# Kernel optimization log

Measured on AMD Instinct MI355X. Metric: run time of the kernel, lower is better.

The kernel has to match this reference:

```python
import math
import jax, jax.numpy as jnp
import numpy as np

B, H, S, D = 2, 16, 2048, 64

def setup_inputs() -> dict:
    key = jax.random.key(0)
    kq, kk, kv = jax.random.split(key, 3)
    return {
        "query": jax.random.normal(kq, (B, H, S, D), dtype=jnp.float32),
        "key": jax.random.normal(kk, (B, H, S, D), dtype=jnp.float32),
        "value": jax.random.normal(kv, (B, H, S, D), dtype=jnp.float32),
        "mask": jnp.ones((B, S, 1), dtype=jnp.float32),  # padding mask, 1 = keep
        "mask_now": 0,  # 0 -> causal (tril diag=0); 1 -> strict causal (diag=-1)
    }

def reference(query, key, value, mask, mask_now):
    d_k = query.shape[-1]
    seq_len = mask.shape[1]
    # [B,H,S,S] scaled scores
    attn_scores = jnp.einsum("bhqd,bhkd->bhqk", query, key) / math.sqrt(d_k)
    diag = -1 if mask_now else 0
    triu_mask = jnp.tril(jnp.ones((seq_len, seq_len), dtype=mask.dtype), diag)  # [S,S]
    # mask[:, :, 0] -> per-query padding mask broadcast over key dim: [B,1,S,S]
    full_mask = triu_mask[None, None, :, :] * mask[:, None, :, 0:1]
    attn_scores = jnp.where(full_mask == 0, jnp.float32(-1e9), attn_scores)
    attn_scores = jax.nn.softmax(attn_scores, axis=-1)
    output = jnp.einsum("bhqk,bhkd->bhqd", attn_scores, value)
    return (output, attn_scores)
```

## Files before the change

kernel.cpp:

```cpp
#include <hip/hip_runtime.h>
#include <math.h>

#define NB 2
#define NH 16
#define SL 2048
#define DD 64
#define NT 256
#define SLABW 268

typedef short bf16x8 __attribute__((ext_vector_type(8)));
typedef float f32x4  __attribute__((ext_vector_type(4)));

__device__ __forceinline__ unsigned short f2bf(float x) {
    unsigned u = __float_as_uint(x);
    u += 0x7fffu + ((u >> 16) & 1u);
    return (unsigned short)(u >> 16);
}

__device__ __forceinline__ void lds_barrier() {
    asm volatile("s_waitcnt lgkmcnt(0)\n\ts_barrier" ::: "memory");
}

__global__ __launch_bounds__(256)
void cvt_bf16(const float* __restrict__ in, unsigned short* __restrict__ out,
              int n4, float scale)
{
    int i = blockIdx.x * 256 + threadIdx.x;
    if (i >= n4) return;
    float4 v = ((const float4*)in)[i];
    ushort4 o;
    o.x = f2bf(v.x * scale); o.y = f2bf(v.y * scale);
    o.z = f2bf(v.z * scale); o.w = f2bf(v.w * scale);
    ((ushort4*)out)[i] = o;
}

__global__ __launch_bounds__(256)
void transpose_v(const float* __restrict__ V, unsigned short* __restrict__ Vt)
{
    __shared__ __align__(16) unsigned short vt[64 * 72];
    const int bh = blockIdx.x >> 5;
    const int s0 = (blockIdx.x & 31) * 64;
    const int t  = threadIdx.x;

    const float4* src = (const float4*)(V + ((size_t)bh * SL + s0) * DD);
    #pragma unroll
    for (int i = 0; i < 4; ++i) {
        int idx = t + i * 256;
        int r = idx >> 4, d4 = idx & 15;
        float4 v = src[r * 16 + d4];
        vt[(d4 * 4 + 0) * 72 + r] = f2bf(v.x);
        vt[(d4 * 4 + 1) * 72 + r] = f2bf(v.y);
        vt[(d4 * 4 + 2) * 72 + r] = f2bf(v.z);
        vt[(d4 * 4 + 3) * 72 + r] = f2bf(v.w);
    }
    __syncthreads();
    const int d = t >> 2, seg = t & 3;
    unsigned short* dst = Vt + ((size_t)bh * DD + d) * SL + s0 + seg * 16;
    uint4 p0 = *(const uint4*)&vt[d * 72 + seg * 16];
    uint4 p1 = *(const uint4*)&vt[d * 72 + seg * 16 + 8];
    *(uint4*)dst = p0;
    *(uint4*)(dst + 8) = p1;
}

__global__ __launch_bounds__(NT, 4)
void attn_mfma(const unsigned short* __restrict__ Qb,
               const unsigned short* __restrict__ Kb,
               const unsigned short* __restrict__ Vt,
               const float* __restrict__ Mg,
               const int* __restrict__ MNg,
               float* __restrict__ Og)
{
    __shared__ __align__(16) float slab[32 * SLABW];
    __shared__ float lsx[4][16];

    const int tid  = threadIdx.x;
    const int w    = tid >> 6;
    const int lane = tid & 63;
    const int l15  = lane & 15;
    const int qd   = lane >> 4;
    const int rowhalf = w >> 1;
    const int colhalf = w & 1;

    const int lin  = blockIdx.x;
    const int xcd  = lin & 7;
    const int iloc = lin >> 3;
    const int g    = iloc & 31;
    const int bh   = xcd * 4 + (iloc >> 5);
    const int b    = bh >> 4;

    const int diag = (MNg[0] != 0) ? -1 : 0;

    const unsigned short* Qh  = Qb + (size_t)bh * SL * DD;
    const unsigned short* Kh  = Kb + (size_t)bh * SL * DD;
    const unsigned short* Vth = Vt + (size_t)bh * DD * SL;
    float* Sb = Og + (size_t)NB * NH * SL * DD + (size_t)bh * SL * SL;
    float* Ob = Og + (size_t)bh * SL * DD;

    for (int sweep = 0; sweep < 2; ++sweep) {
        const int R0 = sweep ? (2016 - g * 32) : (g * 32);

        int degflag = 0;
        if (lane < 32) {
            int row = R0 + lane;
            float m = Mg[(size_t)b * SL + row];
            degflag = (m == 0.0f) || (row + diag < 0);
        }
        const bool deg32 = __any(degflag);
        const int M = deg32 ? 8 : (((R0 + 31 + diag) >> 8) + 1);

        int rlim[4];
        #pragma unroll
        for (int reg = 0; reg < 4; ++reg) {
            int row = R0 + rowhalf * 16 + qd * 4 + reg;
            float m = Mg[(size_t)b * SL + row];
            int rl = row + diag;
            if (m == 0.0f) rl = -1;
            rlim[reg] = rl;
        }

        const unsigned short* qrow = Qh + (size_t)(R0 + rowhalf * 16 + l15) * DD + qd * 8;
        bf16x8 qf0 = *(const bf16x8*)qrow;
        bf16x8 qf1 = *(const bf16x8*)(qrow + 32);

        auto ldK = [&](int ct, bf16x8& f0, bf16x8& f1) {
            const unsigned short* kr = Kh + (size_t)(ct + l15) * DD + qd * 8;
            f0 = *(const bf16x8*)kr;
            f1 = *(const bf16x8*)(kr + 32);
        };

        float lacc[4] = {0.0f, 0.0f, 0.0f, 0.0f};
        {
            auto cmpA = [&](int ct, bf16x8 f0, bf16x8 f1) {
                f32x4 acc = {0.0f, 0.0f, 0.0f, 0.0f};
                __builtin_amdgcn_s_setprio(1);
                acc = __builtin_amdgcn_mfma_f32_16x16x32_bf16(qf0, f0, acc, 0, 0, 0);
                acc = __builtin_amdgcn_mfma_f32_16x16x32_bf16(qf1, f1, acc, 0, 0, 0);
                __builtin_amdgcn_s_setprio(0);
                const int col = ct + l15;
                #pragma unroll
                for (int reg = 0; reg < 4; ++reg)
                    lacc[reg] += (col <= rlim[reg]) ? __builtin_exp2f(acc[reg]) : 0.0f;
            };
            auto tcol = [&](int t) {
                return ((t >> 3) << 8) + colhalf * 128 + ((t & 7) << 4);
            };
            const int T = M * 8;
            bf16x8 A0, A1, B0, B1;
            ldK(tcol(0), A0, A1);
            for (int t = 0; t < T; t += 2) {
                ldK(tcol(t + 1), B0, B1);
                cmpA(tcol(t), A0, A1);
                if (t + 2 < T) ldK(tcol(t + 2), A0, A1);
                cmpA(tcol(t + 1), B0, B1);
            }
        }

        float lsum[4];
        #pragma unroll
        for (int reg = 0; reg < 4; ++reg) {
            float s = lacc[reg];
            s += __shfl_xor(s, 1);  s += __shfl_xor(s, 2);
            s += __shfl_xor(s, 4);  s += __shfl_xor(s, 8);
            lsum[reg] = s;
        }
        if (l15 == 0) {
            #pragma unroll
            for (int reg = 0; reg < 4; ++reg)
                lsx[w][qd * 4 + reg] = lsum[reg];
        }
        lds_barrier();
        float pmul[4], pfill[4];
        #pragma unroll
        for (int reg = 0; reg < 4; ++reg) {
            float tot = lsum[reg] + lsx[w ^ 1][qd * 4 + reg];
            pmul[reg]  = (rlim[reg] < 0) ? 0.0f : 1.0f / tot;
            pfill[reg] = (rlim[reg] < 0) ? (1.0f / (float)SL) : 0.0f;
        }

        f32x4 oacc[2];
        oacc[0] = (f32x4){0.0f, 0.0f, 0.0f, 0.0f};
        oacc[1] = (f32x4){0.0f, 0.0f, 0.0f, 0.0f};

        for (int mc = 0; mc < M; ++mc) {
            const int C0 = mc << 8;
            {
                bf16x8 a0, a1, b0, b1;
                ldK(C0 + colhalf * 128, a0, a1);
                #pragma unroll
                for (int t = 0; t < 8; ++t) {
                    bf16x8 f0 = (t & 1) ? b0 : a0;
                    bf16x8 f1 = (t & 1) ? b1 : a1;
                    if (t < 7) {
                        if (t & 1) ldK(C0 + colhalf * 128 + ((t + 1) << 4), a0, a1);
                        else       ldK(C0 + colhalf * 128 + ((t + 1) << 4), b0, b1);
                    }
                    f32x4 acc = {0.0f, 0.0f, 0.0f, 0.0f};
                    __builtin_amdgcn_s_setprio(1);
                    acc = __builtin_amdgcn_mfma_f32_16x16x32_bf16(qf0, f0, acc, 0, 0, 0);
                    acc = __builtin_amdgcn_mfma_f32_16x16x32_bf16(qf1, f1, acc, 0, 0, 0);
                    __builtin_amdgcn_s_setprio(0);
                    const int scol = colhalf * 128 + (t << 4) + l15;
                    const int col  = C0 + scol;
                    #pragma unroll
                    for (int reg = 0; reg < 4; ++reg) {
                        float val = (col <= rlim[reg]) ? __builtin_exp2f(acc[reg]) * pmul[reg]
                                                       : pfill[reg];
                        slab[(rowhalf * 16 + qd * 4 + reg) * SLABW + scol] = val;
                    }
                }
            }
            lds_barrier();
            #pragma unroll
            for (int i = 0; i < 8; ++i) {
                int rr = w * 8 + i;
                *(float4*)(Sb + (size_t)(R0 + rr) * SL + C0 + lane * 4) =
                    *(const float4*)&slab[rr * SLABW + lane * 4];
            }
            #pragma unroll
            for (int ks = 0; ks < 8; ++ks) {
                const float* pr = &slab[(rowhalf * 16 + l15) * SLABW + ks * 32 + qd * 8];
                float4 x = *(const float4*)pr;
                float4 y = *(const float4*)(pr + 4);
                bf16x8 f;
                f[0] = (short)f2bf(x.x); f[1] = (short)f2bf(x.y);
                f[2] = (short)f2bf(x.z); f[3] = (short)f2bf(x.w);
                f[4] = (short)f2bf(y.x); f[5] = (short)f2bf(y.y);
                f[6] = (short)f2bf(y.z); f[7] = (short)f2bf(y.w);
                #pragma unroll
                for (int nt = 0; nt < 2; ++nt) {
                    const unsigned short* vr = Vth
                        + (size_t)(colhalf * 32 + nt * 16 + l15) * SL + C0 + ks * 32 + qd * 8;
                    bf16x8 v = *(const bf16x8*)vr;
                    __builtin_amdgcn_s_setprio(1);
                    oacc[nt] = __builtin_amdgcn_mfma_f32_16x16x32_bf16(f, v, oacc[nt], 0, 0, 0);
                    __builtin_amdgcn_s_setprio(0);
                }
            }
            lds_barrier();
        }

        {
            const int zc0 = M << 8;
            float4 z = make_float4(0.0f, 0.0f, 0.0f, 0.0f);
            for (int i = 0; i < 8; ++i) {
                float* rowp = Sb + (size_t)(R0 + w * 8 + i) * SL;
                for (int c = zc0 + (lane << 2); c < SL; c += 256)
                    *(float4*)(rowp + c) = z;
            }
        }

        #pragma unroll
        for (int nt = 0; nt < 2; ++nt)
            #pragma unroll
            for (int reg = 0; reg < 4; ++reg)
                slab[(rowhalf * 16 + qd * 4 + reg) * SLABW + colhalf * 32 + nt * 16 + l15] =
                    oacc[nt][reg];
        lds_barrier();
        #pragma unroll
        for (int ii = 0; ii < 2; ++ii) {
            int rr = w * 8 + ii * 4 + (lane >> 4);
            int c4 = lane & 15;
            *(float4*)(Ob + (size_t)(R0 + rr) * DD + c4 * 4) =
                *(const float4*)&slab[rr * SLABW + c4 * 4];
        }
        lds_barrier();
    }
}

extern "C" void kernel_launch(void* const* d_in, const int* in_sizes, int n_in,
                              void* d_out, int out_size, void* d_ws, size_t ws_size,
                              hipStream_t stream)
{
    const float* q  = (const float*)d_in[0];
    const float* k  = (const float*)d_in[1];
    const float* v  = (const float*)d_in[2];
    const float* mk = (const float*)d_in[3];
    const int*   mn = (const int*)d_in[4];
    float* out = (float*)d_out;

    const size_t nElem = (size_t)NB * NH * SL * DD;
    unsigned short* Qb = (unsigned short*)d_ws;
    unsigned short* Kp = Qb + nElem;
    unsigned short* Vp = Kp + nElem;

    const int n4 = (int)(nElem / 4);
    cvt_bf16<<<n4 / 256, 256, 0, stream>>>(q, Qb, n4, 0.125f * 1.44269504f);
    cvt_bf16<<<n4 / 256, 256, 0, stream>>>(k, Kp, n4, 1.0f);
    transpose_v<<<NB * NH * (SL / 64), 256, 0, stream>>>(v, Vp);

    attn_mfma<<<1024, NT, 0, stream>>>(Qb, Kp, Vp, mk, mn, out);
}
```

Before: 735.6 us.

## Stage K and V tiles into swizzled LDS via async global_load_lds with double buffering

Replaces the per-lane direct global loads of K and transposed V with cooperative asynchronous global-to-LDS copies into XOR-swizzled shared buffers. K is double-buffered and prefetched one 64-column chunk ahead. The key-chunk width drops from 256 to 64, which shrinks the score slab and tightens the causal bound to 64-column granularity. The aim is to cut redundant global/L2 traffic and expose more overlap, at the cost of many more barriers per row block and hand-tuned vmcnt waits that could be fragile.

```diff
diff --git a/kernel.cpp b/kernel.cpp
--- a/kernel.cpp
+++ b/kernel.cpp
@@ -5,8 +5,10 @@
 #define NH 16
 #define SL 2048
 #define DD 64
+#define KC 64
+#define NCH (SL / KC)
 #define NT 256
-#define SLABW 268
+#define SLW 68
 
 typedef short bf16x8 __attribute__((ext_vector_type(8)));
 typedef float f32x4  __attribute__((ext_vector_type(4)));
@@ -19,6 +21,12 @@
 
 __device__ __forceinline__ void lds_barrier() {
     asm volatile("s_waitcnt lgkmcnt(0)\n\ts_barrier" ::: "memory");
+}
+
+__device__ __forceinline__ void gl_lds16(const void* src, void* dst) {
+    __builtin_amdgcn_global_load_lds(
+        (const __attribute__((address_space(1))) void*)src,
+        (__attribute__((address_space(3))) void*)dst, 16, 0, 0);
 }
 
 __global__ __launch_bounds__(256)
@@ -70,7 +78,9 @@
                const int* __restrict__ MNg,
                float* __restrict__ Og)
 {
-    __shared__ __align__(16) float slab[32 * SLABW];
+    __shared__ __align__(16) unsigned short kst[2][KC * DD];
+    __shared__ __align__(16) unsigned short vst[DD * KC];
+    __shared__ __align__(16) float slab[32 * SLW];
     __shared__ float lsx[4][16];
 
     const int tid  = threadIdx.x;
@@ -87,7 +97,6 @@
     const int g    = iloc & 31;
     const int bh   = xcd * 4 + (iloc >> 5);
     const int b    = bh >> 4;
-
     const int diag = (MNg[0] != 0) ? -1 : 0;
 
     const unsigned short* Qh  = Qb + (size_t)bh * SL * DD;
@@ -96,6 +105,31 @@
     float* Sb = Og + (size_t)NB * NH * SL * DD + (size_t)bh * SL * SL;
     float* Ob = Og + (size_t)bh * SL * DD;
 
+    const int srw = lane >> 3;
+    const int sc16 = (lane & 7) ^ srw;
+
+    auto stageK = [&](int kc, int dbuf) {
+        const unsigned short* base = Kh + (size_t)kc * KC * DD;
+        #pragma unroll
+        for (int j = 0; j < 2; ++j) {
+            int i = w * 2 + j;
+            const unsigned short* src = base + (size_t)(i * 8 + srw) * DD + sc16 * 8;
+            gl_lds16(src, &kst[dbuf][i * 512]);
+        }
+    };
+    auto stageV = [&](int c0) {
+        #pragma unroll
+        for (int j = 0; j < 2; ++j) {
+            int i = w * 2 + j;
+            const unsigned short* src = Vth + (size_t)(i * 8 + srw) * SL + c0 + sc16 * 8;
+            gl_lds16(src, &vst[i * 512]);
+        }
+    };
+    auto rd16 = [&](const unsigned short* lb, int r, int c16) -> bf16x8 {
+        int a = (r * 128 + c16 * 16) ^ ((r & 7) << 4);
+        return *(const bf16x8*)((const char*)lb + a);
+    };
+
     for (int sweep = 0; sweep < 2; ++sweep) {
         const int R0 = sweep ? (2016 - g * 32) : (g * 32);
 
@@ -106,7 +140,7 @@
             degflag = (m == 0.0f) || (row + diag < 0);
         }
         const bool deg32 = __any(degflag);
-        const int M = deg32 ? 8 : (((R0 + 31 + diag) >> 8) + 1);
+        const int N = deg32 ? NCH : (((R0 + 31 + diag) >> 6) + 1);
 
         int rlim[4];
         #pragma unroll
@@ -122,37 +156,31 @@
         bf16x8 qf0 = *(const bf16x8*)qrow;
         bf16x8 qf1 = *(const bf16x8*)(qrow + 32);
 
-        auto ldK = [&](int ct, bf16x8& f0, bf16x8& f1) {
-            const unsigned short* kr = Kh + (size_t)(ct + l15) * DD + qd * 8;
-            f0 = *(const bf16x8*)kr;
-            f1 = *(const bf16x8*)(kr + 32);
-        };
-
         float lacc[4] = {0.0f, 0.0f, 0.0f, 0.0f};
-        {
-            auto cmpA = [&](int ct, bf16x8 f0, bf16x8 f1) {
+        stageK(0, 0);
+        asm volatile("s_waitcnt vmcnt(0)" ::: "memory");
+        lds_barrier();
+        for (int kc = 0; kc < N; ++kc) {
+            const int d = kc & 1;
+            if (kc + 1 < N) stageK(kc + 1, d ^ 1);
+            const int c0 = kc * KC;
+            #pragma unroll
+            for (int t = 0; t < 2; ++t) {
+                const int ntg = colhalf * 2 + t;
+                bf16x8 b0 = rd16(kst[d], ntg * 16 + l15, qd);
+                bf16x8 b1 = rd16(kst[d], ntg * 16 + l15, 4 + qd);
                 f32x4 acc = {0.0f, 0.0f, 0.0f, 0.0f};
                 __builtin_amdgcn_s_setprio(1);
-                acc = __builtin_amdgcn_mfma_f32_16x16x32_bf16(qf0, f0, acc, 0, 0, 0);
-                acc = __builtin_amdgcn_mfma_f32_16x16x32_bf16(qf1, f1, acc, 0, 0, 0);
+                acc = __builtin_amdgcn_mfma_f32_16x16x32_bf16(qf0, b0, acc, 0, 0, 0);
+                acc = __builtin_amdgcn_mfma_f32_16x16x32_bf16(qf1, b1, acc, 0, 0, 0);
                 __builtin_amdgcn_s_setprio(0);
-                const int col = ct + l15;
+                const int col = c0 + ntg * 16 + l15;
                 #pragma unroll
                 for (int reg = 0; reg < 4; ++reg)
                     lacc[reg] += (col <= rlim[reg]) ? __builtin_exp2f(acc[reg]) : 0.0f;
-            };
-            auto tcol = [&](int t) {
-                return ((t >> 3) << 8) + colhalf * 128 + ((t & 7) << 4);
-            };
-            const int T = M * 8;
-            bf16x8 A0, A1, B0, B1;
-            ldK(tcol(0), A0, A1);
-            for (int t = 0; t < T; t += 2) {
-                ldK(tcol(t + 1), B0, B1);
-                cmpA(tcol(t), A0, A1);
-                if (t + 2 < T) ldK(tcol(t + 2), A0, A1);
-                cmpA(tcol(t + 1), B0, B1);
-            }
+            }
+            asm volatile("s_waitcnt vmcnt(0)" ::: "memory");
+            lds_barrier();
         }
 
         float lsum[4];
@@ -181,44 +209,46 @@
         oacc[0] = (f32x4){0.0f, 0.0f, 0.0f, 0.0f};
         oacc[1] = (f32x4){0.0f, 0.0f, 0.0f, 0.0f};
 
-        for (int mc = 0; mc < M; ++mc) {
-            const int C0 = mc << 8;
-            {
-                bf16x8 a0, a1, b0, b1;
-                ldK(C0 + colhalf * 128, a0, a1);
+        stageK(0, 0);
+        asm volatile("s_waitcnt vmcnt(0)" ::: "memory");
+        lds_barrier();
+        for (int kc = 0; kc < N; ++kc) {
+            const int d  = kc & 1;
+            const int c0 = kc * KC;
+            stageV(c0);
+            const bool pk = (kc + 1 < N);
+            if (pk) stageK(kc + 1, d ^ 1);
+            #pragma unroll
+            for (int t = 0; t < 2; ++t) {
+                const int ntg = colhalf * 2 + t;
+                bf16x8 b0 = rd16(kst[d], ntg * 16 + l15, qd);
+                bf16x8 b1 = rd16(kst[d], ntg * 16 + l15, 4 + qd);
+                f32x4 acc = {0.0f, 0.0f, 0.0f, 0.0f};
+                __builtin_amdgcn_s_setprio(1);
+                acc = __builtin_amdgcn_mfma_f32_16x16x32_bf16(qf0, b0, acc, 0, 0, 0);
+                acc = __builtin_amdgcn_mfma_f32_16x16x32_bf16(qf1, b1, acc, 0, 0, 0);
+                __builtin_amdgcn_s_setprio(0);
+                const int col = c0 + ntg * 16 + l15;
                 #pragma unroll
-                for (int t = 0; t < 8; ++t) {
-                    bf16x8 f0 = (t & 1) ? b0 : a0;
-                    bf16x8 f1 = (t & 1) ? b1 : a1;
-                    if (t < 7) {
-                        if (t & 1) ldK(C0 + colhalf * 128 + ((t + 1) << 4), a0, a1);
-                        else       ldK(C0 + colhalf * 128 + ((t + 1) << 4), b0, b1);
-                    }
-                    f32x4 acc = {0.0f, 0.0f, 0.0f, 0.0f};
-                    __builtin_amdgcn_s_setprio(1);
-                    acc = __builtin_amdgcn_mfma_f32_16x16x32_bf16(qf0, f0, acc, 0, 0, 0);
-                    acc = __builtin_amdgcn_mfma_f32_16x16x32_bf16(qf1, f1, acc, 0, 0, 0);
-                    __builtin_amdgcn_s_setprio(0);
-                    const int scol = colhalf * 128 + (t << 4) + l15;
-                    const int col  = C0 + scol;
-                    #pragma unroll
-                    for (int reg = 0; reg < 4; ++reg) {
-                        float val = (col <= rlim[reg]) ? __builtin_exp2f(acc[reg]) * pmul[reg]
-                                                       : pfill[reg];
-                        slab[(rowhalf * 16 + qd * 4 + reg) * SLABW + scol] = val;
-                    }
+                for (int reg = 0; reg < 4; ++reg) {
+                    float val = (col <= rlim[reg]) ? __builtin_exp2f(acc[reg]) * pmul[reg]
+                                                   : pfill[reg];
+                    slab[(rowhalf * 16 + qd * 4 + reg) * SLW + ntg * 16 + l15] = val;
                 }
             }
+            if (pk) { asm volatile("s_waitcnt vmcnt(2)" ::: "memory"); }
+            else    { asm volatile("s_waitcnt vmcnt(0)" ::: "memory"); }
             lds_barrier();
             #pragma unroll
-            for (int i = 0; i < 8; ++i) {
-                int rr = w * 8 + i;
-                *(float4*)(Sb + (size_t)(R0 + rr) * SL + C0 + lane * 4) =
-                    *(const float4*)&slab[rr * SLABW + lane * 4];
-            }
-            #pragma unroll
-            for (int ks = 0; ks < 8; ++ks) {
-                const float* pr = &slab[(rowhalf * 16 + l15) * SLABW + ks * 32 + qd * 8];
+            for (int ii = 0; ii < 2; ++ii) {
+                int rr = w * 8 + ii * 4 + (lane >> 4);
+                int c4 = lane & 15;
+                *(float4*)(Sb + (size_t)(R0 + rr) * SL + c0 + c4 * 4) =
+                    *(const float4*)&slab[rr * SLW + c4 * 4];
+            }
+            #pragma unroll
+            for (int ks = 0; ks < 2; ++ks) {
+                const float* pr = &slab[(rowhalf * 16 + l15) * SLW + ks * 32 + qd * 8];
                 float4 x = *(const float4*)pr;
                 float4 y = *(const float4*)(pr + 4);
                 bf16x8 f;
@@ -228,19 +258,21 @@
                 f[6] = (short)f2bf(y.z); f[7] = (short)f2bf(y.w);
                 #pragma unroll
                 for (int nt = 0; nt < 2; ++nt) {
-                    const unsigned short* vr = Vth
-                        + (size_t)(colhalf * 32 + nt * 16 + l15) * SL + C0 + ks * 32 + qd * 8;
-                    bf16x8 v = *(const bf16x8*)vr;
+                    bf16x8 v = rd16(vst, colhalf * 32 + nt * 16 + l15, ks * 4 + qd);
                     __builtin_amdgcn_s_setprio(1);
                     oacc[nt] = __builtin_amdgcn_mfma_f32_16x16x32_bf16(f, v, oacc[nt], 0, 0, 0);
                     __builtin_amdgcn_s_setprio(0);
                 }
             }
-            lds_barrier();
-        }
+            if (pk) {
+                asm volatile("s_waitcnt vmcnt(2)" ::: "memory");
+                lds_barrier();
+            }
+        }
+        lds_barrier();
 
         {
-            const int zc0 = M << 8;
+            const int zc0 = N * KC;
             float4 z = make_float4(0.0f, 0.0f, 0.0f, 0.0f);
             for (int i = 0; i < 8; ++i) {
                 float* rowp = Sb + (size_t)(R0 + w * 8 + i) * SL;
@@ -253,7 +285,7 @@
         for (int nt = 0; nt < 2; ++nt)
             #pragma unroll
             for (int reg = 0; reg < 4; ++reg)
-                slab[(rowhalf * 16 + qd * 4 + reg) * SLABW + colhalf * 32 + nt * 16 + l15] =
+                slab[(rowhalf * 16 + qd * 4 + reg) * SLW + colhalf * 32 + nt * 16 + l15] =
                     oacc[nt][reg];
         lds_barrier();
         #pragma unroll
@@ -261,7 +293,7 @@
             int rr = w * 8 + ii * 4 + (lane >> 4);
             int c4 = lane & 15;
             *(float4*)(Ob + (size_t)(R0 + rr) * DD + c4 * 4) =
-                *(const float4*)&slab[rr * SLABW + c4 * 4];
+                *(const float4*)&slab[rr * SLW + c4 * 4];
         }
         lds_barrier();
     }
```

Result: faster. 648.8 us (-11.8%).
